# Kernel optimization log

Hardware: AMD Instinct MI355X
Metric: run time of the kernel (lower is better)

The kernel has to match this reference:

```python
import jax, jax.numpy as jnp
import numpy as np

B, L, D = 8, 2048, 64

def setup_inputs() -> dict:
    key = jax.random.key(0)
    k1, k2 = jax.random.split(key)
    query = jax.random.normal(k1, (B, L, D), dtype=jnp.float32)
    key_t = jax.random.normal(k2, (B, L, D), dtype=jnp.float32)
    return {"query": query, "key": key_t}

def reference(query, key):
    d = query.shape[-1]
    # scores: [B, Lq, Lk] = Q K^T / sqrt(d)
    scores = jnp.einsum('bqd,bkd->bqk', query, key) / jnp.sqrt(jnp.asarray(d, query.dtype))
    weights = jax.nn.softmax(scores, axis=-1)  # dropout p=0.0 -> identity
    # output uses `key` as values, matching the original module
    return jnp.einsum('bqk,bkd->bqd', weights, key)
```

## Files before the change

kernel.cpp:

```cpp
#include <hip/hip_runtime.h>
#include <hip/hip_bf16.h>


#define LL 2048
#define DD 64
#define BQ 128
#define BK 64
#define KPAD 72
#define NSEG 8
#define NQB (LL / BQ)

typedef __attribute__((ext_vector_type(8))) short bf16x8;
typedef __attribute__((ext_vector_type(4))) float f32x4;
typedef __attribute__((ext_vector_type(4))) unsigned short u16x4;

static __device__ __forceinline__ unsigned short f2bf(float f) {
  unsigned u = __builtin_bit_cast(unsigned, f);
  u += 0x7fffu + ((u >> 16) & 1u);
  return (unsigned short)(u >> 16);
}
static __device__ __forceinline__ float bf2f(unsigned short h) {
  unsigned u = (unsigned)h << 16;
  return __builtin_bit_cast(float, u);
}

__global__ __launch_bounds__(256, 3) void attn_kernel(
    const float* __restrict__ Q, const float* __restrict__ K,
    float* __restrict__ O, u16x4* __restrict__ Opart,
    float* __restrict__ Lp, int seglen, int nseg) {
  __shared__ __attribute__((aligned(16))) unsigned short sKt[2][BK][KPAD];
  __shared__ __attribute__((aligned(16))) unsigned short sKtT[2][DD * KPAD];
  __shared__ __attribute__((aligned(16))) unsigned short sP[4][16][KPAD];

  const int tid  = threadIdx.x;
  const int wave = tid >> 6;
  const int lane = tid & 63;
  const int quad = lane >> 4;
  const int l16  = lane & 15;

  const int batch = blockIdx.y;
  const int seg   = blockIdx.z;
  const int q0w   = blockIdx.x * BQ + wave * 32;
  const int ngroups = gridDim.y * NQB;
  const int gq    = batch * NQB + blockIdx.x;

  const float qs = 0.125f * 1.44269504f;
  bf16x8 bq[2][2];
#pragma unroll
  for (int qt = 0; qt < 2; ++qt) {
    const float* qrow = Q + (size_t)(batch * LL + q0w + qt * 16 + l16) * DD;
#pragma unroll
    for (int ks = 0; ks < 2; ++ks) {
      const float* p = qrow + ks * 32 + quad * 8;
      float4 f0 = *(const float4*)(p);
      float4 f1 = *(const float4*)(p + 4);
      bf16x8 a;
      a[0] = (short)f2bf(f0.x * qs); a[1] = (short)f2bf(f0.y * qs);
      a[2] = (short)f2bf(f0.z * qs); a[3] = (short)f2bf(f0.w * qs);
      a[4] = (short)f2bf(f1.x * qs); a[5] = (short)f2bf(f1.y * qs);
      a[6] = (short)f2bf(f1.z * qs); a[7] = (short)f2bf(f1.w * qs);
      bq[qt][ks] = a;
    }
  }

  f32x4 oacc[2][4];
  float l_part[2];
#pragma unroll
  for (int qt = 0; qt < 2; ++qt) {
#pragma unroll
    for (int n = 0; n < 4; ++n) oacc[qt][n] = (f32x4){0.f, 0.f, 0.f, 0.f};
    l_part[qt] = 0.f;
  }

  const int niter = seglen / BK;
  const float* kbase = K + (size_t)(batch * LL + seg * seglen) * DD;

  const int kv_o = tid >> 3;
  const int oc_o = tid & 7;
  const int kv_o2 = (tid + 256) >> 3;

  float4 pf[2][2];
#pragma unroll
  for (int i = 0; i < 2; ++i) {
    int p = tid + i * 256;
    const float4* src = (const float4*)(kbase + (size_t)(p >> 3) * DD + (p & 7) * 8);
    pf[i][0] = src[0];
    pf[i][1] = src[1];
  }
#pragma unroll
  for (int i = 0; i < 2; ++i) {
    int kv = i ? kv_o2 : kv_o, oc = oc_o;
    unsigned short h[8];
    h[0] = f2bf(pf[i][0].x); h[1] = f2bf(pf[i][0].y);
    h[2] = f2bf(pf[i][0].z); h[3] = f2bf(pf[i][0].w);
    h[4] = f2bf(pf[i][1].x); h[5] = f2bf(pf[i][1].y);
    h[6] = f2bf(pf[i][1].z); h[7] = f2bf(pf[i][1].w);
    *(bf16x8*)&sKt[0][kv][oc * 8] = *(const bf16x8*)h;
    int swz = ((kv >> 3) ^ oc) & 7;
    unsigned short* dst = &sKtT[0][(oc * 8) * KPAD + swz * 8 + (kv & 7)];
#pragma unroll
    for (int j = 0; j < 8; ++j) dst[j * KPAD] = h[j];
  }
  __syncthreads();

  for (int t = 0; t < niter; ++t) {
    const int cur = t & 1;
    const int nxt = cur ^ 1;

    if (t + 1 < niter) {
      const float* kt = kbase + (size_t)(t + 1) * BK * DD;
#pragma unroll
      for (int i = 0; i < 2; ++i) {
        int p = tid + i * 256;
        const float4* src = (const float4*)(kt + (size_t)(p >> 3) * DD + (p & 7) * 8);
        pf[i][0] = src[0];
        pf[i][1] = src[1];
      }
    }

    f32x4 s[2][4];
#pragma unroll
    for (int mt = 0; mt < 4; ++mt) {
      bf16x8 k0 = *(const bf16x8*)&sKt[cur][mt * 16 + l16][quad * 8];
      bf16x8 k1 = *(const bf16x8*)&sKt[cur][mt * 16 + l16][32 + quad * 8];
      f32x4 z = (f32x4){0.f, 0.f, 0.f, 0.f};
      s[0][mt] = __builtin_amdgcn_mfma_f32_16x16x32_bf16(k0, bq[0][0], z, 0, 0, 0);
      s[0][mt] = __builtin_amdgcn_mfma_f32_16x16x32_bf16(k1, bq[0][1], s[0][mt], 0, 0, 0);
      s[1][mt] = __builtin_amdgcn_mfma_f32_16x16x32_bf16(k0, bq[1][0], z, 0, 0, 0);
      s[1][mt] = __builtin_amdgcn_mfma_f32_16x16x32_bf16(k1, bq[1][1], s[1][mt], 0, 0, 0);
    }

    bf16x8 bfr[2][4];
#pragma unroll
    for (int ks = 0; ks < 2; ++ks)
#pragma unroll
      for (int nt = 0; nt < 4; ++nt) {
        int d = nt * 16 + l16;
        bfr[ks][nt] = *(const bf16x8*)
            &sKtT[cur][d * KPAD + (((ks * 4 + quad) ^ (d >> 3)) & 7) * 8];
      }

#pragma unroll
    for (int qt = 0; qt < 2; ++qt) {
#pragma unroll
      for (int mt = 0; mt < 4; ++mt) {
        u16x4 h;
#pragma unroll
        for (int r = 0; r < 4; ++r) {
          float p = __builtin_amdgcn_exp2f(s[qt][mt][r]);
          l_part[qt] += p;
          h[r] = f2bf(p);
        }
        *(u16x4*)&sP[wave][l16][mt * 16 + quad * 4] = h;
      }
      bf16x8 a0 = *(const bf16x8*)&sP[wave][l16][quad * 8];
      bf16x8 a1 = *(const bf16x8*)&sP[wave][l16][32 + quad * 8];
#pragma unroll
      for (int nt = 0; nt < 4; ++nt) {
        oacc[qt][nt] = __builtin_amdgcn_mfma_f32_16x16x32_bf16(a0, bfr[0][nt], oacc[qt][nt], 0, 0, 0);
        oacc[qt][nt] = __builtin_amdgcn_mfma_f32_16x16x32_bf16(a1, bfr[1][nt], oacc[qt][nt], 0, 0, 0);
      }
    }

    if (t + 1 < niter) {
#pragma unroll
      for (int i = 0; i < 2; ++i) {
        int kv = i ? kv_o2 : kv_o, oc = oc_o;
        unsigned short h[8];
        h[0] = f2bf(pf[i][0].x); h[1] = f2bf(pf[i][0].y);
        h[2] = f2bf(pf[i][0].z); h[3] = f2bf(pf[i][0].w);
        h[4] = f2bf(pf[i][1].x); h[5] = f2bf(pf[i][1].y);
        h[6] = f2bf(pf[i][1].z); h[7] = f2bf(pf[i][1].w);
        *(bf16x8*)&sKt[nxt][kv][oc * 8] = *(const bf16x8*)h;
        int swz = ((kv >> 3) ^ oc) & 7;
        unsigned short* dst = &sKtT[nxt][(oc * 8) * KPAD + swz * 8 + (kv & 7)];
#pragma unroll
        for (int j = 0; j < 8; ++j) dst[j * KPAD] = h[j];
      }
    }
    __syncthreads();
  }

#pragma unroll
  for (int qt = 0; qt < 2; ++qt) {
    l_part[qt] += __shfl_xor(l_part[qt], 16);
    l_part[qt] += __shfl_xor(l_part[qt], 32);
  }

  if (nseg == 1) {
#pragma unroll
    for (int qt = 0; qt < 2; ++qt)
#pragma unroll
      for (int r = 0; r < 4; ++r) {
        float lr = __shfl(l_part[qt], (lane & 48) | (quad * 4 + r), 64);
        float invl = 1.0f / lr;
        float* orow = O + (size_t)(batch * LL + q0w + qt * 16 + quad * 4 + r) * DD;
#pragma unroll
        for (int nt = 0; nt < 4; ++nt)
          orow[nt * 16 + l16] = oacc[qt][nt][r] * invl;
      }
    return;
  }

  const size_t slotbase = ((size_t)seg * ngroups + gq) * 32 + wave * 8;
#pragma unroll
  for (int qt = 0; qt < 2; ++qt) {
#pragma unroll
    for (int nt = 0; nt < 4; ++nt) {
      u16x4 h;
      h[0] = f2bf(oacc[qt][nt][0]); h[1] = f2bf(oacc[qt][nt][1]);
      h[2] = f2bf(oacc[qt][nt][2]); h[3] = f2bf(oacc[qt][nt][3]);
      Opart[(slotbase + qt * 4 + nt) * 64 + lane] = h;
    }
    if (quad == 0)
      Lp[(((size_t)seg * ngroups + gq) * 8 + wave * 2 + qt) * 16 + l16] = l_part[qt];
  }
}

__global__ __launch_bounds__(256) void combine_kernel(
    const u16x4* __restrict__ Opart, const float* __restrict__ Lp,
    float* __restrict__ O, int nseg, int ngroups) {
  const int tid  = threadIdx.x;
  const int g    = blockIdx.x;
  const int slot = blockIdx.y * 4 + (tid >> 6);
  const int lane = tid & 63;
  const int quad = lane >> 4;
  const int l16  = lane & 15;
  const int wv = slot >> 3, qt = (slot >> 2) & 1, nt = slot & 3;

  f32x4 acc = (f32x4){0.f, 0.f, 0.f, 0.f};
  float den = 0.f;
  for (int s = 0; s < nseg; ++s) {
    u16x4 h = Opart[((size_t)(s * ngroups + g) * 32 + slot) * 64 + lane];
    acc[0] += bf2f(h[0]); acc[1] += bf2f(h[1]);
    acc[2] += bf2f(h[2]); acc[3] += bf2f(h[3]);
    den += Lp[((size_t)(s * ngroups + g) * 8 + wv * 2 + qt) * 16 + l16];
  }
  const int batch = g / NQB, qbx = g % NQB;
  const int rowbase = batch * LL + qbx * BQ + wv * 32 + qt * 16;
#pragma unroll
  for (int r = 0; r < 4; ++r) {
    float dr = __shfl(den, (lane & 48) | (quad * 4 + r), 64);
    O[(size_t)(rowbase + quad * 4 + r) * DD + nt * 16 + l16] = acc[r] / dr;
  }
}

extern "C" void kernel_launch(void* const* d_in, const int* in_sizes, int n_in,
                              void* d_out, int out_size, void* d_ws, size_t ws_size,
                              hipStream_t stream) {
  const float* Q = (const float*)d_in[0];
  const float* K = (const float*)d_in[1];
  float* O = (float*)d_out;
  int B = in_sizes[0] / (LL * DD);
  int ngroups = B * NQB;

  size_t opart_bytes = (size_t)NSEG * ngroups * 32 * 64 * sizeof(u16x4);
  size_t lp_bytes    = (size_t)NSEG * ngroups * 8 * 16 * sizeof(float);
  if (ws_size >= opart_bytes + lp_bytes) {
    u16x4* Opart = (u16x4*)d_ws;
    float* Lpp = (float*)((char*)d_ws + opart_bytes);
    dim3 grid(NQB, B, NSEG);
    attn_kernel<<<grid, 256, 0, stream>>>(Q, K, O, Opart, Lpp, LL / NSEG, NSEG);
    combine_kernel<<<dim3(ngroups, 8), 256, 0, stream>>>(Opart, Lpp, O, NSEG, ngroups);
  } else {
    dim3 grid(NQB, B, 1);
    attn_kernel<<<grid, 256, 0, stream>>>(Q, K, O, nullptr, nullptr, LL, 1);
  }
}
```

Baseline: 90.28 us.

## Single-buffer K tiles in LDS and raise occupancy to four blocks

Replaces the double-buffered K and transposed-K shared-memory tiles with single buffers, roughly halving LDS per block, and raises the launch-bounds minimum from 3 to 4 blocks per CU. Each iteration now loads all P and K^T fragments into registers, synchronises, writes the next K tile into the same buffer, then runs the PV MFMAs so they overlap the LDS stores. This adds a second barrier per iteration and keeps more fragments live in registers, which may cause spills under the tighter register budget.

```diff
diff --git a/kernel.cpp b/kernel.cpp
--- a/kernel.cpp
+++ b/kernel.cpp
@@ -24,12 +24,12 @@
   return __builtin_bit_cast(float, u);
 }
 
-__global__ __launch_bounds__(256, 3) void attn_kernel(
+__global__ __launch_bounds__(256, 4) void attn_kernel(
     const float* __restrict__ Q, const float* __restrict__ K,
     float* __restrict__ O, u16x4* __restrict__ Opart,
     float* __restrict__ Lp, int seglen, int nseg) {
-  __shared__ __attribute__((aligned(16))) unsigned short sKt[2][BK][KPAD];
-  __shared__ __attribute__((aligned(16))) unsigned short sKtT[2][DD * KPAD];
+  __shared__ __attribute__((aligned(16))) unsigned short sKt[BK][KPAD];
+  __shared__ __attribute__((aligned(16))) unsigned short sKtT[DD * KPAD];
   __shared__ __attribute__((aligned(16))) unsigned short sP[4][16][KPAD];
 
   const int tid  = threadIdx.x;
@@ -74,9 +74,8 @@
 
   const int niter = seglen / BK;
   const float* kbase = K + (size_t)(batch * LL + seg * seglen) * DD;
-
-  const int kv_o = tid >> 3;
-  const int oc_o = tid & 7;
+  const int kv_o  = tid >> 3;
+  const int oc_o  = tid & 7;
   const int kv_o2 = (tid + 256) >> 3;
 
   float4 pf[2][2];
@@ -95,18 +94,15 @@
     h[2] = f2bf(pf[i][0].z); h[3] = f2bf(pf[i][0].w);
     h[4] = f2bf(pf[i][1].x); h[5] = f2bf(pf[i][1].y);
     h[6] = f2bf(pf[i][1].z); h[7] = f2bf(pf[i][1].w);
-    *(bf16x8*)&sKt[0][kv][oc * 8] = *(const bf16x8*)h;
+    *(bf16x8*)&sKt[kv][oc * 8] = *(const bf16x8*)h;
     int swz = ((kv >> 3) ^ oc) & 7;
-    unsigned short* dst = &sKtT[0][(oc * 8) * KPAD + swz * 8 + (kv & 7)];
+    unsigned short* dst = &sKtT[(oc * 8) * KPAD + swz * 8 + (kv & 7)];
 #pragma unroll
     for (int j = 0; j < 8; ++j) dst[j * KPAD] = h[j];
   }
   __syncthreads();
 
   for (int t = 0; t < niter; ++t) {
-    const int cur = t & 1;
-    const int nxt = cur ^ 1;
-
     if (t + 1 < niter) {
       const float* kt = kbase + (size_t)(t + 1) * BK * DD;
 #pragma unroll
@@ -121,8 +117,8 @@
     f32x4 s[2][4];
 #pragma unroll
     for (int mt = 0; mt < 4; ++mt) {
-      bf16x8 k0 = *(const bf16x8*)&sKt[cur][mt * 16 + l16][quad * 8];
-      bf16x8 k1 = *(const bf16x8*)&sKt[cur][mt * 16 + l16][32 + quad * 8];
+      bf16x8 k0 = *(const bf16x8*)&sKt[mt * 16 + l16][quad * 8];
+      bf16x8 k1 = *(const bf16x8*)&sKt[mt * 16 + l16][32 + quad * 8];
       f32x4 z = (f32x4){0.f, 0.f, 0.f, 0.f};
       s[0][mt] = __builtin_amdgcn_mfma_f32_16x16x32_bf16(k0, bq[0][0], z, 0, 0, 0);
       s[0][mt] = __builtin_amdgcn_mfma_f32_16x16x32_bf16(k1, bq[0][1], s[0][mt], 0, 0, 0);
@@ -130,16 +126,7 @@
       s[1][mt] = __builtin_amdgcn_mfma_f32_16x16x32_bf16(k1, bq[1][1], s[1][mt], 0, 0, 0);
     }
 
-    bf16x8 bfr[2][4];
-#pragma unroll
-    for (int ks = 0; ks < 2; ++ks)
-#pragma unroll
-      for (int nt = 0; nt < 4; ++nt) {
-        int d = nt * 16 + l16;
-        bfr[ks][nt] = *(const bf16x8*)
-            &sKtT[cur][d * KPAD + (((ks * 4 + quad) ^ (d >> 3)) & 7) * 8];
-      }
-
+    bf16x8 pa[2][2];
 #pragma unroll
     for (int qt = 0; qt < 2; ++qt) {
 #pragma unroll
@@ -153,14 +140,21 @@
         }
         *(u16x4*)&sP[wave][l16][mt * 16 + quad * 4] = h;
       }
-      bf16x8 a0 = *(const bf16x8*)&sP[wave][l16][quad * 8];
-      bf16x8 a1 = *(const bf16x8*)&sP[wave][l16][32 + quad * 8];
+      pa[qt][0] = *(const bf16x8*)&sP[wave][l16][quad * 8];
+      pa[qt][1] = *(const bf16x8*)&sP[wave][l16][32 + quad * 8];
+    }
+
+    bf16x8 bfr[2][4];
+#pragma unroll
+    for (int ks = 0; ks < 2; ++ks)
 #pragma unroll
       for (int nt = 0; nt < 4; ++nt) {
-        oacc[qt][nt] = __builtin_amdgcn_mfma_f32_16x16x32_bf16(a0, bfr[0][nt], oacc[qt][nt], 0, 0, 0);
-        oacc[qt][nt] = __builtin_amdgcn_mfma_f32_16x16x32_bf16(a1, bfr[1][nt], oacc[qt][nt], 0, 0, 0);
-      }
-    }
+        int d = nt * 16 + l16;
+        bfr[ks][nt] = *(const bf16x8*)
+            &sKtT[d * KPAD + (((ks * 4 + quad) ^ (d >> 3)) & 7) * 8];
+      }
+
+    __syncthreads();
 
     if (t + 1 < niter) {
 #pragma unroll
@@ -171,13 +165,22 @@
         h[2] = f2bf(pf[i][0].z); h[3] = f2bf(pf[i][0].w);
         h[4] = f2bf(pf[i][1].x); h[5] = f2bf(pf[i][1].y);
         h[6] = f2bf(pf[i][1].z); h[7] = f2bf(pf[i][1].w);
-        *(bf16x8*)&sKt[nxt][kv][oc * 8] = *(const bf16x8*)h;
+        *(bf16x8*)&sKt[kv][oc * 8] = *(const bf16x8*)h;
         int swz = ((kv >> 3) ^ oc) & 7;
-        unsigned short* dst = &sKtT[nxt][(oc * 8) * KPAD + swz * 8 + (kv & 7)];
+        unsigned short* dst = &sKtT[(oc * 8) * KPAD + swz * 8 + (kv & 7)];
 #pragma unroll
         for (int j = 0; j < 8; ++j) dst[j * KPAD] = h[j];
       }
     }
+
+#pragma unroll
+    for (int qt = 0; qt < 2; ++qt)
+#pragma unroll
+      for (int nt = 0; nt < 4; ++nt) {
+        oacc[qt][nt] = __builtin_amdgcn_mfma_f32_16x16x32_bf16(pa[qt][0], bfr[0][nt], oacc[qt][nt], 0, 0, 0);
+        oacc[qt][nt] = __builtin_amdgcn_mfma_f32_16x16x32_bf16(pa[qt][1], bfr[1][nt], oacc[qt][nt], 0, 0, 0);
+      }
+
     __syncthreads();
   }
 
```

New measurement: 138.0 us. 52.8% more time.
